# Kernel tuning notes

Measured on AMD Instinct MI355X. Metric: run time of the kernel, lower is better.

## Reference

```python
import jax, jax.numpy as jnp
import numpy as np

N = 100000   # total nodes
E = 600000   # total edges
G = 2048     # graphs in batch
DIN = 9      # input node feature dim
D = 128      # hidden == output dim
L = 5        # GIN layers
BN_EPS = 1e-5
LN_EPS = 1e-5


def setup_inputs() -> dict:
    key = jax.random.key(0)
    ks = jax.random.split(key, 24)
    s = 0.05
    x = jax.random.normal(ks[0], (N, DIN), jnp.float32)
    edge_index = jax.random.randint(ks[1], (2, E), 0, N, dtype=jnp.int32)
    batch = jnp.sort(jax.random.randint(ks[2], (N,), 0, G, dtype=jnp.int32))
    return {
        "x": x,
        "edge_index": edge_index,
        "batch": batch,
        # node embedding
        "node_emb_W": jax.random.normal(ks[3], (DIN, D), jnp.float32) * s,
        "node_emb_b": jnp.zeros((D,), jnp.float32),
        # GIN layer MLPs, stacked over layers: Linear(D,2D) -> ReLU -> Linear(2D,D)
        "W1s": jax.random.normal(ks[4], (L, D, 2 * D), jnp.float32) * s,
        "b1s": jnp.zeros((L, 2 * D), jnp.float32),
        "W2s": jax.random.normal(ks[5], (L, 2 * D, D), jnp.float32) * s,
        "b2s": jnp.zeros((L, D), jnp.float32),
        # BatchNorm affine params per layer
        "bn_g": jnp.ones((L, D), jnp.float32),
        "bn_b": jnp.zeros((L, D), jnp.float32),
        # virtual node
        "vn_emb": jax.random.normal(ks[6], (1, D), jnp.float32),
        "vn_W1": jax.random.normal(ks[7], (D, D), jnp.float32) * s,
        "vn_b1": jnp.zeros((D,), jnp.float32),
        "vn_W2": jax.random.normal(ks[8], (D, D), jnp.float32) * s,
        "vn_b2": jnp.zeros((D,), jnp.float32),
        # graph MLP: Linear -> LayerNorm -> ReLU -> Linear
        "gm_W1": jax.random.normal(ks[9], (D, D), jnp.float32) * s,
        "gm_b1": jnp.zeros((D,), jnp.float32),
        "ln_g": jnp.ones((D,), jnp.float32),
        "ln_b": jnp.zeros((D,), jnp.float32),
        "gm_W2": jax.random.normal(ks[10], (D, D), jnp.float32) * s,
        "gm_b2": jnp.zeros((D,), jnp.float32),
    }


def _mean_pool(h, batch):
    # segment mean over graphs: [N, D] -> [G, D]
    s = jax.ops.segment_sum(h, batch, num_segments=G)
    cnt = jax.ops.segment_sum(jnp.ones((h.shape[0], 1), h.dtype), batch, num_segments=G)
    return s / jnp.maximum(cnt, 1.0)


def _batchnorm(m, g, b):
    mu = jnp.mean(m, axis=0)
    var = jnp.mean(jnp.square(m - mu), axis=0)  # biased var (torch train-mode norm)
    return (m - mu) * jax.lax.rsqrt(var + BN_EPS) * g + b


def reference(x, edge_index, batch, node_emb_W, node_emb_b, W1s, b1s, W2s, b2s,
              bn_g, bn_b, vn_emb, vn_W1, vn_b1, vn_W2, vn_b2,
              gm_W1, gm_b1, ln_g, ln_b, gm_W2, gm_b2):
    src, dst = edge_index[0], edge_index[1]
    h = x @ node_emb_W + node_emb_b                       # [N, D]
    vn = jnp.tile(vn_emb, (G, 1))                         # [G, D]
    for i in range(L):
        h_prev = h
        # GINConv (eps=0): mlp(h + sum_{j->i} h_j) via gather/scatter-add
        agg = jax.ops.segment_sum(h[src], dst, num_segments=N)
        m = h + agg
        m = jax.nn.relu(m @ W1s[i] + b1s[i]) @ W2s[i] + b2s[i]
        h = jax.nn.relu(_batchnorm(m, bn_g[i], bn_b[i]))
        # (dropout is identity in eval mode)
        if i > 0:
            h = h + h_prev
        # virtual node: pool -> MLP -> broadcast back
        temp = _mean_pool(h, batch)                       # [G, D]
        vn = vn + (jax.nn.relu(temp @ vn_W1 + vn_b1) @ vn_W2 + vn_b2)
        h = h + vn[batch]
    node_features = h                                     # output_projection = Identity
    gf = _mean_pool(node_features, batch)                 # [G, D]
    gf = gf @ gm_W1 + gm_b1
    mu = jnp.mean(gf, axis=-1, keepdims=True)
    var = jnp.mean(jnp.square(gf - mu), axis=-1, keepdims=True)
    gf = (gf - mu) * jax.lax.rsqrt(var + LN_EPS) * ln_g + ln_b
    gf = jax.nn.relu(gf)
    graph_features = gf @ gm_W2 + gm_b2
    return node_features, graph_features
```

## Files before the change

### kernel.cpp

```cpp
#include <hip/hip_runtime.h>
#include <stdint.h>

#define NNODES 100000
#define NEDGES 600000
#define NGRAPH 2048
#define DD 128
#define NLAYER 5
#define NPAD 100096
#define SCAN_NB 391
#define NSTAT 32
#define MAXROWS 128

typedef __attribute__((ext_vector_type(8))) __bf16 bf16x8;
typedef __attribute__((ext_vector_type(4))) float f32x4;
typedef __attribute__((ext_vector_type(8))) ushort u16x8;

__device__ __forceinline__ ushort f2b(float f) {
    union { float f; uint32_t u; } v; v.f = f;
    uint32_t r = v.u + 0x7FFFu + ((v.u >> 16) & 1u);
    return (ushort)(r >> 16);
}

__device__ __forceinline__ float b2f(ushort u) {
    union { uint32_t u; float f; } v; v.u = ((uint32_t)u) << 16; return v.f;
}

__device__ __forceinline__ void gload_lds16(const void* g, void* l) {
    __builtin_amdgcn_global_load_lds(
        (const __attribute__((address_space(1))) void*)g,
        (__attribute__((address_space(3))) void*)l, 16, 0, 0);
}

__global__ void prep_w_kernel(const float* __restrict__ W1s, const float* __restrict__ W2s,
                              ushort* __restrict__ w1t, ushort* __restrict__ w2t) {
    int idx = blockIdx.x * 256 + threadIdx.x;
    const int per = 128 * 256;
    if (idx < NLAYER * per) {
        int i = idx / per, rem = idx % per;
        int n = rem >> 7, k = rem & 127;
        w1t[idx] = f2b(W1s[(size_t)i * per + k * 256 + n]);
    } else if (idx < 2 * NLAYER * per) {
        int j = idx - NLAYER * per;
        int i = j / per, rem = j % per;
        int n = rem >> 8, k = rem & 255;
        w2t[j] = f2b(W2s[(size_t)i * per + k * 128 + n]);
    }
}

__global__ void node_embed_kernel(const float* __restrict__ x, const float* __restrict__ W,
                                  const float* __restrict__ b, ushort* __restrict__ hb,
                                  const float* __restrict__ vne, float* __restrict__ vn) {
    int idx = blockIdx.x * 256 + threadIdx.x;
    if (idx < NNODES * 128) {
        int n = idx >> 7, d = idx & 127;
        float v = b[d];
#pragma unroll
        for (int k = 0; k < 9; ++k) v += x[n * 9 + k] * W[k * 128 + d];
        hb[(size_t)n * 128 + d] = f2b(v);
    } else if (idx < NNODES * 128 + NGRAPH * 128) {
        int r = idx - NNODES * 128;
        vn[r] = vne[r & 127];
    }
}


__global__ void deg_kernel(const int* __restrict__ dst, int* __restrict__ deg) {
    int e = blockIdx.x * 256 + threadIdx.x;
    if (e < NEDGES) atomicAdd(&deg[dst[e]], 1);
}

__global__ void scan_part_kernel(const int* __restrict__ deg, int* __restrict__ partials) {
    int i = blockIdx.x * 256 + threadIdx.x;
    int lane = threadIdx.x & 63, w = threadIdx.x >> 6;
    int v = (i < NNODES) ? deg[i] : 0;
#pragma unroll
    for (int o = 1; o < 64; o <<= 1) v += __shfl_xor(v, o);
    __shared__ int ws[4];
    if (lane == 0) ws[w] = v;
    __syncthreads();
    if (threadIdx.x == 0) partials[blockIdx.x] = ws[0] + ws[1] + ws[2] + ws[3];
}

__global__ __launch_bounds__(512)
void scan_top_kernel(int* __restrict__ partials) {
    __shared__ int s[512];
    int t = threadIdx.x;
    int v = (t < SCAN_NB) ? partials[t] : 0;
    s[t] = v;
    __syncthreads();
#pragma unroll
    for (int o = 1; o < 512; o <<= 1) {
        int n = (t >= o) ? s[t - o] : 0;
        __syncthreads();
        s[t] += n;
        __syncthreads();
    }
    if (t < SCAN_NB) partials[t] = s[t] - v;
}

__global__ void scan_blocks_kernel(const int* __restrict__ deg, const int* __restrict__ partials,
                                   int* __restrict__ rs, int* __restrict__ cursor) {
    int i = blockIdx.x * 256 + threadIdx.x;
    int lane = threadIdx.x & 63, w = threadIdx.x >> 6;
    int v = (i < NNODES) ? deg[i] : 0;
    int x = v;
#pragma unroll
    for (int o = 1; o < 64; o <<= 1) {
        int n = __shfl_up(x, o);
        if (lane >= o) x += n;
    }
    __shared__ int ws[4];
    if (lane == 63) ws[w] = x;
    __syncthreads();
    if (threadIdx.x == 0) {
        int a = 0;
#pragma unroll
        for (int k = 0; k < 4; ++k) { int t = ws[k]; ws[k] = a; a += t; }
    }
    __syncthreads();
    int excl = (x - v) + ws[w] + partials[blockIdx.x];
    if (i < NNODES) { rs[i] = excl; cursor[i] = excl; }
    if (i == 0) rs[NNODES] = NEDGES;
}

__global__ void csr_scatter_kernel(const int* __restrict__ src, const int* __restrict__ dst,
                                   int* __restrict__ cursor, int* __restrict__ csrc) {
    int e = blockIdx.x * 256 + threadIdx.x;
    if (e < NEDGES) {
        int p = atomicAdd(&cursor[dst[e]], 1);
        csrc[p] = src[e];
    }
}

__device__ __forceinline__ int lbound(const int* __restrict__ b, int key) {
    int lo = 0, hi = NNODES;
    while (lo < hi) { int m = (lo + hi) >> 1; if (b[m] < key) lo = m + 1; else hi = m; }
    return lo;
}

__global__ void gstart_kernel(const int* __restrict__ batch, int* __restrict__ gstart,
                              float* __restrict__ inv) {
    int g = blockIdx.x * 256 + threadIdx.x;
    if (g <= NGRAPH)
        gstart[g] = (g == NGRAPH) ? NNODES : lbound(batch, g);
    if (g < NGRAPH) {
        int c = lbound(batch, g + 1) - lbound(batch, g);
        inv[g] = 1.f / (float)(c > 0 ? c : 1);
    }
}


__global__ __launch_bounds__(256)
void gin_agg_kernel(const ushort* __restrict__ hb, const int* __restrict__ rs,
                    const int* __restrict__ csrc, ushort* __restrict__ xb,
                    float* __restrict__ stats) {
    if (blockIdx.x < NSTAT) stats[blockIdx.x * 256 + threadIdx.x] = 0.f;
    int slot = threadIdx.x >> 4;
    int j = threadIdx.x & 15;
    int node = blockIdx.x * 16 + slot;
    if (node >= NNODES) return;
    int s = rs[node], e = rs[node + 1];
    u16x8 v0 = *(const u16x8*)(hb + (size_t)node * 128 + j * 8);
    float a[8], b[8];
#pragma unroll
    for (int t = 0; t < 8; ++t) { a[t] = b2f(v0[t]); b[t] = 0.f; }
    int k = s;
    for (; k + 3 < e; k += 4) {
        int s0 = csrc[k], s1 = csrc[k + 1], s2 = csrc[k + 2], s3 = csrc[k + 3];
        u16x8 va = *(const u16x8*)(hb + (size_t)s0 * 128 + j * 8);
        u16x8 vb = *(const u16x8*)(hb + (size_t)s1 * 128 + j * 8);
        u16x8 vc = *(const u16x8*)(hb + (size_t)s2 * 128 + j * 8);
        u16x8 vd = *(const u16x8*)(hb + (size_t)s3 * 128 + j * 8);
#pragma unroll
        for (int t = 0; t < 8; ++t) {
            a[t] += b2f(va[t]) + b2f(vc[t]);
            b[t] += b2f(vb[t]) + b2f(vd[t]);
        }
    }
    for (; k < e; ++k) {
        int s0 = csrc[k];
        u16x8 va = *(const u16x8*)(hb + (size_t)s0 * 128 + j * 8);
#pragma unroll
        for (int t = 0; t < 8; ++t) a[t] += b2f(va[t]);
    }
    u16x8 o;
#pragma unroll
    for (int t = 0; t < 8; ++t) o[t] = f2b(a[t] + b[t]);
    *(u16x8*)(xb + (size_t)node * 128 + j * 8) = o;
}

#define MLP_TILES 4
#define MLP_GRID 391
__global__ __launch_bounds__(256, 2)
void fused_mlp_kernel(const ushort* __restrict__ A, const ushort* __restrict__ W1,
                      const float* __restrict__ b1, const ushort* __restrict__ W2,
                      const float* __restrict__ b2, ushort* __restrict__ out_b,
                      float* __restrict__ stats) {
    __shared__ __align__(16) ushort lA[8192];
    __shared__ __align__(16) ushort mid[16384];
    const int tid = threadIdx.x;
    const int lane = tid & 63, w = tid >> 6;
    const int q = lane >> 4, l16 = lane & 15;
    float* sbase = stats + (blockIdx.x & (NSTAT - 1)) * 256;

    bf16x8 w1f[4][4], w2f[8][2];
#pragma unroll
    for (int ks = 0; ks < 4; ++ks)
#pragma unroll
        for (int ni = 0; ni < 4; ++ni)
            w1f[ks][ni] = *(const bf16x8*)(W1 + (size_t)(w * 64 + ni * 16 + l16) * 128 + ks * 32 + q * 8);
#pragma unroll
    for (int ks = 0; ks < 8; ++ks)
#pragma unroll
        for (int ni = 0; ni < 2; ++ni)
            w2f[ks][ni] = *(const bf16x8*)(W2 + (size_t)(w * 32 + ni * 16 + l16) * 256 + ks * 32 + q * 8);

    {
        int rb = blockIdx.x * (64 * MLP_TILES);
#pragma unroll
        for (int p = 0; p < 4; ++p)
            gload_lds16(A + (size_t)(rb + lane) * 128 + p * 32 + w * 8,
                        &lA[(size_t)(p * 256 + w * 64 + lane) * 8]);
    }

    for (int tt = 0; tt < MLP_TILES; ++tt) {
        const int rb = blockIdx.x * (64 * MLP_TILES) + tt * 64;
        __syncthreads();

        f32x4 acc1[4][4] = {};
#pragma unroll
        for (int ks = 0; ks < 4; ++ks) {
            bf16x8 af[4];
#pragma unroll
            for (int mi = 0; mi < 4; ++mi)
                af[mi] = *(const bf16x8*)&lA[ks * 2048 + q * 512 + (mi * 16 + l16) * 8];
#pragma unroll
            for (int mi = 0; mi < 4; ++mi)
#pragma unroll
                for (int ni = 0; ni < 4; ++ni)
                    acc1[mi][ni] = __builtin_amdgcn_mfma_f32_16x16x32_bf16(af[mi], w1f[ks][ni], acc1[mi][ni], 0, 0, 0);
        }

#pragma unroll
        for (int ni = 0; ni < 4; ++ni) {
            int col = w * 64 + ni * 16 + l16;
            float bs = b1[col];
            int g2 = col >> 3, jj = col & 7;
#pragma unroll
            for (int mi = 0; mi < 4; ++mi) {
                int rowb = mi * 16 + q * 4;
#pragma unroll
                for (int r = 0; r < 4; ++r) {
                    float v = acc1[mi][ni][r] + bs;
                    v = v > 0.f ? v : 0.f;
                    mid[g2 * 512 + (rowb + r) * 8 + jj] = f2b(v);
                }
            }
        }
        __syncthreads();

        if (tt + 1 < MLP_TILES) {
            int rb2 = rb + 64;
#pragma unroll
            for (int p = 0; p < 4; ++p)
                gload_lds16(A + (size_t)(rb2 + lane) * 128 + p * 32 + w * 8,
                            &lA[(size_t)(p * 256 + w * 64 + lane) * 8]);
        }

        f32x4 acc2[4][2] = {};
#pragma unroll
        for (int ks = 0; ks < 8; ++ks) {
            bf16x8 af[4];
#pragma unroll
            for (int mi = 0; mi < 4; ++mi)
                af[mi] = *(const bf16x8*)&mid[(ks * 4 + q) * 512 + (mi * 16 + l16) * 8];
#pragma unroll
            for (int mi = 0; mi < 4; ++mi)
#pragma unroll
                for (int ni = 0; ni < 2; ++ni)
                    acc2[mi][ni] = __builtin_amdgcn_mfma_f32_16x16x32_bf16(af[mi], w2f[ks][ni], acc2[mi][ni], 0, 0, 0);
        }

#pragma unroll
        for (int ni = 0; ni < 2; ++ni) {
            int col = w * 32 + ni * 16 + l16;
            float bs = b2[col];
            float s = 0.f, sq = 0.f;
#pragma unroll
            for (int mi = 0; mi < 4; ++mi) {
                int row = rb + mi * 16 + q * 4;
#pragma unroll
                for (int r = 0; r < 4; ++r) {
                    float v = acc2[mi][ni][r] + bs;
                    out_b[(size_t)(row + r) * 128 + col] = f2b(v);
                    if (row + r < NNODES) { s += v; sq += v * v; }
                }
            }
            s  += __shfl_xor(s, 16);  s  += __shfl_xor(s, 32);
            sq += __shfl_xor(sq, 16); sq += __shfl_xor(sq, 32);
            if (lane < 16) {
                atomicAdd(&sbase[col], s);
                atomicAdd(&sbase[128 + col], sq);
            }
        }
    }
}

template<int FINAL>
__global__ __launch_bounds__(256)
void tail_kernel(const ushort* __restrict__ m, ushort* __restrict__ hb,
                 const float* __restrict__ stats,
                 const float* __restrict__ bng, const float* __restrict__ bnb,
                 const int* __restrict__ gstart, const float* __restrict__ inv,
                 const float* __restrict__ W1, const float* __restrict__ b1,
                 const float* __restrict__ W2, const float* __restrict__ b2,
                 float* __restrict__ vn, float* __restrict__ outN, int resid) {
    __shared__ __align__(16) ushort rowbuf[MAXROWS * 128];
    __shared__ float sC[128], sS[128];
    __shared__ float red[16][128];
    __shared__ float t[128], t1[128], vns[128];
    int g = blockIdx.x, tid = threadIdx.x;
    if (tid < 128) {
        int d = tid;
        float sum = 0.f, sq = 0.f;
#pragma unroll
        for (int c = 0; c < NSTAT; ++c) {
            sum += stats[c * 256 + d];
            sq  += stats[c * 256 + 128 + d];
        }
        float mu = sum * (1.f / NNODES);
        float var = sq * (1.f / NNODES) - mu * mu;
        var = var < 0.f ? 0.f : var;
        float sc = bng[d] * rsqrtf(var + 1e-5f);
        sC[d] = sc;
        sS[d] = bnb[d] - mu * sc;
    }
    __syncthreads();
    int j = tid & 15, rg = tid >> 4;
    float sc8[8], sh8[8], acc[8];
#pragma unroll
    for (int k = 0; k < 8; ++k) { sc8[k] = sC[j * 8 + k]; sh8[k] = sS[j * 8 + k]; acc[k] = 0.f; }
    int s = gstart[g], e = gstart[g + 1];

    for (int r = s + rg; r < e; r += 16) {
        u16x8 mv = *(const u16x8*)(m + (size_t)r * 128 + j * 8);
        float v[8];
#pragma unroll
        for (int k = 0; k < 8; ++k) v[k] = fmaxf(b2f(mv[k]) * sc8[k] + sh8[k], 0.f);
        if (resid) {
            u16x8 hv = *(const u16x8*)(hb + (size_t)r * 128 + j * 8);
#pragma unroll
            for (int k = 0; k < 8; ++k) v[k] += b2f(hv[k]);
        }
#pragma unroll
        for (int k = 0; k < 8; ++k) acc[k] += v[k];
        int idx = r - s;
        if (idx < MAXROWS) {
            u16x8 o;
#pragma unroll
            for (int k = 0; k < 8; ++k) o[k] = f2b(v[k]);
            *(u16x8*)(rowbuf + idx * 128 + j * 8) = o;
        }
    }
#pragma unroll
    for (int k = 0; k < 8; ++k) red[rg][j * 8 + k] = acc[k];
    __syncthreads();
    if (tid < 128) {
        int d = tid;
        float tot = 0.f;
#pragma unroll
        for (int r2 = 0; r2 < 16; ++r2) tot += red[r2][d];
        t[d] = tot * inv[g];
    }
    __syncthreads();
    if (tid < 128) {
        int d = tid;
        float a = b1[d];
        for (int k = 0; k < 128; ++k) a += t[k] * W1[k * 128 + d];
        t1[d] = fmaxf(a, 0.f);
    }
    __syncthreads();
    if (tid < 128) {
        int d = tid;
        float o = b2[d];
        for (int k = 0; k < 128; ++k) o += t1[k] * W2[k * 128 + d];
        float vnew = vn[(size_t)g * 128 + d] + o;
        vn[(size_t)g * 128 + d] = vnew;
        vns[d] = vnew;
    }
    __syncthreads();

    float vg[8];
#pragma unroll
    for (int k = 0; k < 8; ++k) vg[k] = vns[j * 8 + k];

    for (int r = s + rg; r < e; r += 16) {
        int idx = r - s;
        float v[8];
        if (idx < MAXROWS) {
            u16x8 wv = *(const u16x8*)(rowbuf + idx * 128 + j * 8);
#pragma unroll
            for (int k = 0; k < 8; ++k) v[k] = b2f(wv[k]);
        } else {
            u16x8 mv = *(const u16x8*)(m + (size_t)r * 128 + j * 8);
#pragma unroll
            for (int k = 0; k < 8; ++k) v[k] = fmaxf(b2f(mv[k]) * sc8[k] + sh8[k], 0.f);
            if (resid) {
                u16x8 hv = *(const u16x8*)(hb + (size_t)r * 128 + j * 8);
#pragma unroll
                for (int k = 0; k < 8; ++k) v[k] += b2f(hv[k]);
            }
        }
#pragma unroll
        for (int k = 0; k < 8; ++k) v[k] += vg[k];
        u16x8 o;
#pragma unroll
        for (int k = 0; k < 8; ++k) o[k] = f2b(v[k]);
        *(u16x8*)(hb + (size_t)r * 128 + j * 8) = o;
        if (FINAL) {
            float4* op = (float4*)(outN + (size_t)r * 128 + j * 8);
            op[0] = make_float4(v[0], v[1], v[2], v[3]);
            op[1] = make_float4(v[4], v[5], v[6], v[7]);
        }
    }
}

__global__ __launch_bounds__(256)
void graph_mlp_kernel(const ushort* __restrict__ hb, const int* __restrict__ gstart,
                      const float* __restrict__ inv,
                      const float* __restrict__ W1, const float* __restrict__ b1,
                      const float* __restrict__ lng, const float* __restrict__ lnb,
                      const float* __restrict__ W2, const float* __restrict__ b2,
                      float* __restrict__ out) {
    __shared__ float red[16][128];
    __shared__ float t[128], t1[128], lred[2];
    int g = blockIdx.x, tid = threadIdx.x;
    int j = tid & 15, rg = tid >> 4;
    float acc[8];
#pragma unroll
    for (int k = 0; k < 8; ++k) acc[k] = 0.f;
    int s = gstart[g], e = gstart[g + 1];
    for (int r = s + rg; r < e; r += 16) {
        u16x8 hv = *(const u16x8*)(hb + (size_t)r * 128 + j * 8);
#pragma unroll
        for (int k = 0; k < 8; ++k) acc[k] += b2f(hv[k]);
    }
#pragma unroll
    for (int k = 0; k < 8; ++k) red[rg][j * 8 + k] = acc[k];
    __syncthreads();
    if (tid < 128) {
        int d = tid;
        float tot = 0.f;
#pragma unroll
        for (int r2 = 0; r2 < 16; ++r2) tot += red[r2][d];
        t[d] = tot * inv[g];
    }
    __syncthreads();
    float a = 0.f, dv = 0.f;
    if (tid < 128) {
        int d = tid;
        a = b1[d];
        for (int k = 0; k < 128; ++k) a += t[k] * W1[k * 128 + d];
        int lane = d & 63, w = d >> 6;
        float ssum = a;
#pragma unroll
        for (int o = 1; o < 64; o <<= 1) ssum += __shfl_xor(ssum, o);
        if (lane == 0) lred[w] = ssum;
    }
    __syncthreads();
    if (tid < 128) {
        int d = tid;
        int lane = d & 63, w = d >> 6;
        float mu = (lred[0] + lred[1]) * (1.f / 128.f);
        dv = a - mu;
        float qq = dv * dv;
#pragma unroll
        for (int o = 1; o < 64; o <<= 1) qq += __shfl_xor(qq, o);
        if (lane == 0) lred[w] = qq;
    }
    __syncthreads();
    if (tid < 128) {
        int d = tid;
        float var = (lred[0] + lred[1]) * (1.f / 128.f);
        float v = dv * rsqrtf(var + 1e-5f) * lng[d] + lnb[d];
        t1[d] = fmaxf(v, 0.f);
    }
    __syncthreads();
    if (tid < 128) {
        int d = tid;
        float o2 = b2[d];
        for (int k = 0; k < 128; ++k) o2 += t1[k] * W2[k * 128 + d];
        out[g * 128 + d] = o2;
    }
}

extern "C" void kernel_launch(void* const* d_in, const int* in_sizes, int n_in,
                              void* d_out, int out_size, void* d_ws, size_t ws_size,
                              hipStream_t stream) {
    const float* x    = (const float*)d_in[0];
    const int*   edge = (const int*)d_in[1];
    const int*   src  = edge;
    const int*   dst  = edge + NEDGES;
    const int*   batch = (const int*)d_in[2];
    const float* nW   = (const float*)d_in[3];
    const float* nb   = (const float*)d_in[4];
    const float* W1s  = (const float*)d_in[5];
    const float* b1s  = (const float*)d_in[6];
    const float* W2s  = (const float*)d_in[7];
    const float* b2s  = (const float*)d_in[8];
    const float* bng  = (const float*)d_in[9];
    const float* bnb  = (const float*)d_in[10];
    const float* vne  = (const float*)d_in[11];
    const float* vW1  = (const float*)d_in[12];
    const float* vb1  = (const float*)d_in[13];
    const float* vW2  = (const float*)d_in[14];
    const float* vb2  = (const float*)d_in[15];
    const float* gW1  = (const float*)d_in[16];
    const float* gb1  = (const float*)d_in[17];
    const float* lng  = (const float*)d_in[18];
    const float* lnb  = (const float*)d_in[19];
    const float* gW2  = (const float*)d_in[20];
    const float* gb2  = (const float*)d_in[21];

    char* ws = (char*)d_ws;
    auto alloc = [&](size_t bytes) { char* p = ws; ws += (bytes + 255) & ~(size_t)255; return p; };
    float*  stats = (float*)alloc((size_t)NSTAT * 256 * 4);
    ushort* hb    = (ushort*)alloc((size_t)NPAD * 128 * 2);
    ushort* mbuf  = (ushort*)alloc((size_t)NPAD * 128 * 2);
    ushort* xb    = (ushort*)alloc((size_t)NPAD * 128 * 2);
    float*  vn    = (float*)alloc((size_t)NGRAPH * 128 * 4);
    ushort* w1t   = (ushort*)alloc((size_t)NLAYER * 256 * 128 * 2);
    ushort* w2t   = (ushort*)alloc((size_t)NLAYER * 128 * 256 * 2);
    float*  inv   = (float*)alloc((size_t)NGRAPH * 4);
    int*    gstart= (int*)alloc((size_t)(NGRAPH + 1) * 4);
    int*    deg   = (int*)alloc((size_t)NNODES * 4);
    int*    rs    = (int*)alloc((size_t)(NNODES + 1) * 4);
    int*    cursor= (int*)alloc((size_t)NNODES * 4);
    int*    csrc  = (int*)alloc((size_t)NEDGES * 4);
    int*    partials = (int*)alloc((size_t)SCAN_NB * 4);

    float* outN = (float*)d_out;
    float* outG = outN + (size_t)NNODES * 128;

    hipMemsetAsync(stats, 0, (size_t)NSTAT * 256 * 4, stream);
    hipMemsetAsync(deg, 0, (size_t)NNODES * 4, stream);

    deg_kernel<<<(NEDGES + 255) / 256, 256, 0, stream>>>(dst, deg);
    scan_part_kernel<<<SCAN_NB, 256, 0, stream>>>(deg, partials);
    scan_top_kernel<<<1, 512, 0, stream>>>(partials);
    scan_blocks_kernel<<<SCAN_NB, 256, 0, stream>>>(deg, partials, rs, cursor);
    csr_scatter_kernel<<<(NEDGES + 255) / 256, 256, 0, stream>>>(src, dst, cursor, csrc);
    gstart_kernel<<<(NGRAPH + 256) / 256, 256, 0, stream>>>(batch, gstart, inv);

    prep_w_kernel<<<(2 * NLAYER * 128 * 256 + 255) / 256, 256, 0, stream>>>(W1s, W2s, w1t, w2t);
    node_embed_kernel<<<((NNODES + NGRAPH) * 128 + 255) / 256, 256, 0, stream>>>(
        x, nW, nb, hb, vne, vn);

    for (int i = 0; i < NLAYER; ++i) {
        gin_agg_kernel<<<(NNODES + 15) / 16, 256, 0, stream>>>(hb, rs, csrc, xb, stats);
        fused_mlp_kernel<<<MLP_GRID, 256, 0, stream>>>(
            xb, w1t + (size_t)i * 256 * 128, b1s + i * 256,
            w2t + (size_t)i * 128 * 256, b2s + i * 128, mbuf, stats);
        if (i < NLAYER - 1)
            tail_kernel<0><<<NGRAPH, 256, 0, stream>>>(
                mbuf, hb, stats, bng + i * 128, bnb + i * 128, gstart, inv,
                vW1, vb1, vW2, vb2, vn, nullptr, i > 0 ? 1 : 0);
        else
            tail_kernel<1><<<NGRAPH, 256, 0, stream>>>(
                mbuf, hb, stats, bng + i * 128, bnb + i * 128, gstart, inv,
                vW1, vb1, vW2, vb2, vn, outN, 1);
    }
    graph_mlp_kernel<<<NGRAPH, 256, 0, stream>>>(hb, gstart, inv, gW1, gb1, lng, lnb, gW2, gb2, outG);
}
```

Measured before the change: 595.7 us.

## Drop LDS row cache, compute final graph pool algebraically in tail kernel

```diff
diff --git a/kernel.cpp b/kernel.cpp
--- a/kernel.cpp
+++ b/kernel.cpp
@@ -9,7 +9,6 @@
 #define NPAD 100096
 #define SCAN_NB 391
 #define NSTAT 32
-#define MAXROWS 128
 
 typedef __attribute__((ext_vector_type(8))) __bf16 bf16x8;
 typedef __attribute__((ext_vector_type(4))) float f32x4;
@@ -314,8 +313,8 @@
                  const int* __restrict__ gstart, const float* __restrict__ inv,
                  const float* __restrict__ W1, const float* __restrict__ b1,
                  const float* __restrict__ W2, const float* __restrict__ b2,
-                 float* __restrict__ vn, float* __restrict__ outN, int resid) {
-    __shared__ __align__(16) ushort rowbuf[MAXROWS * 128];
+                 float* __restrict__ vn, float* __restrict__ outN,
+                 float* __restrict__ gf, int resid) {
     __shared__ float sC[128], sS[128];
     __shared__ float red[16][128];
     __shared__ float t[128], t1[128], vns[128];
@@ -354,13 +353,6 @@
         }
 #pragma unroll
         for (int k = 0; k < 8; ++k) acc[k] += v[k];
-        int idx = r - s;
-        if (idx < MAXROWS) {
-            u16x8 o;
-#pragma unroll
-            for (int k = 0; k < 8; ++k) o[k] = f2b(v[k]);
-            *(u16x8*)(rowbuf + idx * 128 + j * 8) = o;
-        }
     }
 #pragma unroll
     for (int k = 0; k < 8; ++k) red[rg][j * 8 + k] = acc[k];
@@ -387,6 +379,7 @@
         float vnew = vn[(size_t)g * 128 + d] + o;
         vn[(size_t)g * 128 + d] = vnew;
         vns[d] = vnew;
+        if (FINAL) gf[(size_t)g * 128 + d] = (e > s) ? (t[d] + vnew) : 0.f;
     }
     __syncthreads();
 
@@ -395,103 +388,64 @@
     for (int k = 0; k < 8; ++k) vg[k] = vns[j * 8 + k];
 
     for (int r = s + rg; r < e; r += 16) {
-        int idx = r - s;
+        u16x8 mv = *(const u16x8*)(m + (size_t)r * 128 + j * 8);
         float v[8];
-        if (idx < MAXROWS) {
-            u16x8 wv = *(const u16x8*)(rowbuf + idx * 128 + j * 8);
-#pragma unroll
-            for (int k = 0; k < 8; ++k) v[k] = b2f(wv[k]);
-        } else {
-            u16x8 mv = *(const u16x8*)(m + (size_t)r * 128 + j * 8);
-#pragma unroll
-            for (int k = 0; k < 8; ++k) v[k] = fmaxf(b2f(mv[k]) * sc8[k] + sh8[k], 0.f);
-            if (resid) {
-                u16x8 hv = *(const u16x8*)(hb + (size_t)r * 128 + j * 8);
-#pragma unroll
-                for (int k = 0; k < 8; ++k) v[k] += b2f(hv[k]);
-            }
+#pragma unroll
+        for (int k = 0; k < 8; ++k) v[k] = fmaxf(b2f(mv[k]) * sc8[k] + sh8[k], 0.f);
+        if (resid) {
+            u16x8 hv = *(const u16x8*)(hb + (size_t)r * 128 + j * 8);
+#pragma unroll
+            for (int k = 0; k < 8; ++k) v[k] += b2f(hv[k]);
         }
 #pragma unroll
         for (int k = 0; k < 8; ++k) v[k] += vg[k];
-        u16x8 o;
-#pragma unroll
-        for (int k = 0; k < 8; ++k) o[k] = f2b(v[k]);
-        *(u16x8*)(hb + (size_t)r * 128 + j * 8) = o;
         if (FINAL) {
             float4* op = (float4*)(outN + (size_t)r * 128 + j * 8);
             op[0] = make_float4(v[0], v[1], v[2], v[3]);
             op[1] = make_float4(v[4], v[5], v[6], v[7]);
-        }
-    }
-}
-
-__global__ __launch_bounds__(256)
-void graph_mlp_kernel(const ushort* __restrict__ hb, const int* __restrict__ gstart,
-                      const float* __restrict__ inv,
+        } else {
+            u16x8 o;
+#pragma unroll
+            for (int k = 0; k < 8; ++k) o[k] = f2b(v[k]);
+            *(u16x8*)(hb + (size_t)r * 128 + j * 8) = o;
+        }
+    }
+}
+
+__global__ __launch_bounds__(128)
+void graph_mlp_kernel(const float* __restrict__ gf,
                       const float* __restrict__ W1, const float* __restrict__ b1,
                       const float* __restrict__ lng, const float* __restrict__ lnb,
                       const float* __restrict__ W2, const float* __restrict__ b2,
                       float* __restrict__ out) {
-    __shared__ float red[16][128];
     __shared__ float t[128], t1[128], lred[2];
-    int g = blockIdx.x, tid = threadIdx.x;
-    int j = tid & 15, rg = tid >> 4;
-    float acc[8];
-#pragma unroll
-    for (int k = 0; k < 8; ++k) acc[k] = 0.f;
-    int s = gstart[g], e = gstart[g + 1];
-    for (int r = s + rg; r < e; r += 16) {
-        u16x8 hv = *(const u16x8*)(hb + (size_t)r * 128 + j * 8);
-#pragma unroll
-        for (int k = 0; k < 8; ++k) acc[k] += b2f(hv[k]);
-    }
-#pragma unroll
-    for (int k = 0; k < 8; ++k) red[rg][j * 8 + k] = acc[k];
-    __syncthreads();
-    if (tid < 128) {
-        int d = tid;
-        float tot = 0.f;
-#pragma unroll
-        for (int r2 = 0; r2 < 16; ++r2) tot += red[r2][d];
-        t[d] = tot * inv[g];
-    }
-    __syncthreads();
-    float a = 0.f, dv = 0.f;
-    if (tid < 128) {
-        int d = tid;
-        a = b1[d];
-        for (int k = 0; k < 128; ++k) a += t[k] * W1[k * 128 + d];
-        int lane = d & 63, w = d >> 6;
-        float ssum = a;
-#pragma unroll
-        for (int o = 1; o < 64; o <<= 1) ssum += __shfl_xor(ssum, o);
-        if (lane == 0) lred[w] = ssum;
-    }
-    __syncthreads();
-    if (tid < 128) {
-        int d = tid;
-        int lane = d & 63, w = d >> 6;
-        float mu = (lred[0] + lred[1]) * (1.f / 128.f);
-        dv = a - mu;
-        float qq = dv * dv;
-#pragma unroll
-        for (int o = 1; o < 64; o <<= 1) qq += __shfl_xor(qq, o);
-        if (lane == 0) lred[w] = qq;
-    }
-    __syncthreads();
-    if (tid < 128) {
-        int d = tid;
-        float var = (lred[0] + lred[1]) * (1.f / 128.f);
-        float v = dv * rsqrtf(var + 1e-5f) * lng[d] + lnb[d];
-        t1[d] = fmaxf(v, 0.f);
-    }
-    __syncthreads();
-    if (tid < 128) {
-        int d = tid;
-        float o2 = b2[d];
-        for (int k = 0; k < 128; ++k) o2 += t1[k] * W2[k * 128 + d];
-        out[g * 128 + d] = o2;
-    }
+    int g = blockIdx.x, d = threadIdx.x;
+    int lane = d & 63, w = d >> 6;
+    t[d] = gf[(size_t)g * 128 + d];
+    __syncthreads();
+    float a = b1[d];
+    for (int k = 0; k < 128; ++k) a += t[k] * W1[k * 128 + d];
+    float ssum = a;
+#pragma unroll
+    for (int o = 1; o < 64; o <<= 1) ssum += __shfl_xor(ssum, o);
+    if (lane == 0) lred[w] = ssum;
+    __syncthreads();
+    float mu = (lred[0] + lred[1]) * (1.f / 128.f);
+    float dv = a - mu;
+    float qq = dv * dv;
+#pragma unroll
+    for (int o = 1; o < 64; o <<= 1) qq += __shfl_xor(qq, o);
+    __syncthreads();
+    if (lane == 0) lred[w] = qq;
+    __syncthreads();
+    float var = (lred[0] + lred[1]) * (1.f / 128.f);
+    float v = dv * rsqrtf(var + 1e-5f) * lng[d] + lnb[d];
+    v = fmaxf(v, 0.f);
+    t1[d] = v;
+    __syncthreads();
+    float o2 = b2[d];
+    for (int k = 0; k < 128; ++k) o2 += t1[k] * W2[k * 128 + d];
+    out[g * 128 + d] = o2;
 }
 
 extern "C" void kernel_launch(void* const* d_in, const int* in_sizes, int n_in,
@@ -529,6 +483,7 @@
     ushort* mbuf  = (ushort*)alloc((size_t)NPAD * 128 * 2);
     ushort* xb    = (ushort*)alloc((size_t)NPAD * 128 * 2);
     float*  vn    = (float*)alloc((size_t)NGRAPH * 128 * 4);
+    float*  gf    = (float*)alloc((size_t)NGRAPH * 128 * 4);
     ushort* w1t   = (ushort*)alloc((size_t)NLAYER * 256 * 128 * 2);
     ushort* w2t   = (ushort*)alloc((size_t)NLAYER * 128 * 256 * 2);
     float*  inv   = (float*)alloc((size_t)NGRAPH * 4);
@@ -564,11 +519,11 @@
         if (i < NLAYER - 1)
             tail_kernel<0><<<NGRAPH, 256, 0, stream>>>(
                 mbuf, hb, stats, bng + i * 128, bnb + i * 128, gstart, inv,
-                vW1, vb1, vW2, vb2, vn, nullptr, i > 0 ? 1 : 0);
+                vW1, vb1, vW2, vb2, vn, nullptr, nullptr, i > 0 ? 1 : 0);
         else
             tail_kernel<1><<<NGRAPH, 256, 0, stream>>>(
                 mbuf, hb, stats, bng + i * 128, bnb + i * 128, gstart, inv,
-                vW1, vb1, vW2, vb2, vn, outN, 1);
-    }
-    graph_mlp_kernel<<<NGRAPH, 256, 0, stream>>>(hb, gstart, inv, gW1, gb1, lng, lnb, gW2, gb2, outG);
-}
+                vW1, vb1, vW2, vb2, vn, outN, gf, 1);
+    }
+    graph_mlp_kernel<<<NGRAPH, 128, 0, stream>>>(gf, gW1, gb1, lng, lnb, gW2, gb2, outG);
+}
```

After: 576.1 us. 1.03x faster.
